# Kernel tuning notes

Hardware: AMD Instinct MI355X
Metric: run time of the kernel (lower is better)

## Reference

```python
import jax, jax.numpy as jnp
import numpy as np

QKV = 1024   # qkv_size (input feature dim)
E = 64       # embed_size (per-head dim)
H = 16       # num_heads
OUT = 1024   # output_size
B, S = 8, 1024


def setup_inputs() -> dict:
    key = jax.random.key(0)
    ks = jax.random.split(key, 8)
    inv = 1.0 / np.sqrt(QKV)
    return {
        "query": jax.random.normal(ks[0], (B, S, QKV), jnp.float32),
        "key": jax.random.normal(ks[1], (B, S, QKV), jnp.float32),
        "value": jax.random.normal(ks[2], (B, S, QKV), jnp.float32),
        # stacked per-head projection weights, torch Linear convention y = x @ W.T -> store as [H, QKV, E]
        "Wq": jax.random.normal(ks[3], (H, QKV, E), jnp.float32) * inv,
        "Wk": jax.random.normal(ks[4], (H, QKV, E), jnp.float32) * inv,
        "Wv": jax.random.normal(ks[5], (H, QKV, E), jnp.float32) * inv,
        "Wo": jax.random.normal(ks[6], (OUT, H * E), jnp.float32) / np.sqrt(H * E),
        "bo": jax.random.normal(ks[7], (OUT,), jnp.float32) * 0.01,
    }


def reference(query, key, value, Wq, Wk, Wv, Wo, bo):
    # batched over heads: [B,S,QKV] x [H,QKV,E] -> [B,H,S,E]
    Q = jnp.einsum("bsd,hde->bhse", query, Wq)
    K = jnp.einsum("bsd,hde->bhse", key, Wk)
    V = jnp.einsum("bsd,hde->bhse", value, Wv)
    # NOTE: original scales by sqrt(qkv_dim) (input dim), not per-head dim
    scale = 1.0 / jnp.sqrt(jnp.float32(QKV))
    scores = jnp.einsum("bhse,bhte->bhst", Q, K) * scale  # [B,H,S,S]
    attn = jax.nn.softmax(scores, axis=-1)
    attended = jnp.einsum("bhst,bhte->bhse", attn, V)     # [B,H,S,E]
    # concat heads along last dim (head-major order matches torch.cat of head outputs)
    concat = attended.transpose(0, 2, 1, 3).reshape(query.shape[0], query.shape[1], H * E)
    return concat @ Wo.T + bo
```

## Files before the change

### kernel.cpp

```cpp
#include <hip/hip_runtime.h>
#include <stdint.h>


typedef __bf16 bf16x8 __attribute__((ext_vector_type(8)));
typedef float f32x4 __attribute__((ext_vector_type(4)));

typedef __attribute__((address_space(3))) uint32_t lds_u32;
typedef const __attribute__((address_space(1))) uint32_t glb_u32;

__device__ __forceinline__ ushort f2bf(float f) {
  uint32_t x = __float_as_uint(f);
  x += 0x7fff + ((x >> 16) & 1);
  return (ushort)(x >> 16);
}
__device__ __forceinline__ bf16x8 ld8(const ushort* p) {
  union { uint4 u; bf16x8 b; } c;
  c.u = *reinterpret_cast<const uint4*>(p);
  return c.b;
}
__device__ __forceinline__ void cvt16(const float* __restrict__ src,
                                      ushort* __restrict__ dst) {
  union { uint4 u[2]; ushort s[16]; } o;
#pragma unroll
  for (int i = 0; i < 4; ++i) {
    const float4 f = reinterpret_cast<const float4*>(src)[i];
    o.s[4 * i + 0] = f2bf(f.x);
    o.s[4 * i + 1] = f2bf(f.y);
    o.s[4 * i + 2] = f2bf(f.z);
    o.s[4 * i + 3] = f2bf(f.w);
  }
  reinterpret_cast<uint4*>(dst)[0] = o.u[0];
  reinterpret_cast<uint4*>(dst)[1] = o.u[1];
}

__device__ __forceinline__ void gld16(const ushort* g, ushort* l) {
  __builtin_amdgcn_global_load_lds((glb_u32*)g, (lds_u32*)l, 16, 0, 0);
}

__global__ __launch_bounds__(256) void prep_wt(const float* __restrict__ W,
                                               ushort* __restrict__ WT) {
  __shared__ __align__(16) ushort tile[64 * 72];
  const int h = blockIdx.x >> 4;
  const int kt = blockIdx.x & 15;
  const int t = threadIdx.x;
  const int row = t >> 2;
  const int ch = (t & 3) * 16;
  cvt16(W + ((size_t)h * 1024 + kt * 64 + row) * 64 + ch, &tile[row * 72 + ch]);
  __syncthreads();
  const int e = t >> 2;
  const int kc = (t & 3) * 16;
  ushort vals[16];
#pragma unroll
  for (int j = 0; j < 16; ++j) vals[j] = tile[(kc + j) * 72 + e];
  ushort* dst = WT + (size_t)(h * 64 + e) * 1024 + kt * 64 + kc;
  reinterpret_cast<uint4*>(dst)[0] = *reinterpret_cast<uint4*>(&vals[0]);
  reinterpret_cast<uint4*>(dst)[1] = *reinterpret_cast<uint4*>(&vals[8]);
}

__global__ __launch_bounds__(256) void cvt_wo(const float* __restrict__ src,
                                              ushort* __restrict__ dst) {
  const int i = (blockIdx.x * 256 + threadIdx.x) * 16;
  cvt16(src + i, dst + i);
}

__global__ __launch_bounds__(256) void cvt2(const float* __restrict__ s0,
                                            ushort* __restrict__ d0,
                                            const float* __restrict__ s1,
                                            ushort* __restrict__ d1) {
  const int b = blockIdx.x;
  const float* s = (b < 2048) ? s0 : s1;
  ushort* d = (b < 2048) ? d0 : d1;
  const int i = ((b & 2047) * 256 + threadIdx.x) * 16;
  cvt16(s + i, d + i);
}

template <bool F32OUT>
__device__ __forceinline__ void gemm_core(const ushort* __restrict__ A,
                                          const ushort* __restrict__ Bt,
                                          const float* __restrict__ bias,
                                          void* __restrict__ Cv, float oscale,
                                          int bx, int by) {
  __shared__ __align__(16) ushort As[128 * 64];
  __shared__ __align__(16) ushort Bs[128 * 64];
  const int n0 = bx * 128;
  const int m0 = by * 128;
  const int t = threadIdx.x;
  const int lane = t & 63;
  const int w = t >> 6;
  const int wm = w >> 1, wn = w & 1;
  const int col = lane & 15;
  const int quad = lane >> 4;
  const int gr = lane >> 3;
  const int gc = (lane & 7) * 8;

  f32x4 acc[4][4];
#pragma unroll
  for (int i = 0; i < 4; ++i)
#pragma unroll
    for (int j = 0; j < 4; ++j) acc[i][j] = (f32x4){0.f, 0.f, 0.f, 0.f};

  const ushort* a_src = A + (size_t)(m0 + w * 8 + gr) * 1024 + gc;
  const ushort* b_src = Bt + (size_t)(n0 + w * 8 + gr) * 1024 + gc;
  ushort* as_base = &As[(w * 8) * 64];
  ushort* bs_base = &Bs[(w * 8) * 64];

  for (int k0 = 0; k0 < 1024; k0 += 64) {
#pragma unroll
    for (int c = 0; c < 4; ++c) {
      gld16(a_src + (size_t)c * 32 * 1024 + k0, as_base + c * 32 * 64);
      gld16(b_src + (size_t)c * 32 * 1024 + k0, bs_base + c * 32 * 64);
    }
    __syncthreads();

#pragma unroll
    for (int half = 0; half < 2; ++half) {
      bf16x8 af[4], bfr[4];
#pragma unroll
      for (int i = 0; i < 4; ++i)
        af[i] = ld8(&As[(wm * 64 + i * 16 + col) * 64 + half * 32 + quad * 8]);
#pragma unroll
      for (int j = 0; j < 4; ++j)
        bfr[j] = ld8(&Bs[(wn * 64 + j * 16 + col) * 64 + half * 32 + quad * 8]);
#pragma unroll
      for (int i = 0; i < 4; ++i)
#pragma unroll
        for (int j = 0; j < 4; ++j)
          acc[i][j] = __builtin_amdgcn_mfma_f32_16x16x32_bf16(af[i], bfr[j],
                                                              acc[i][j], 0, 0, 0);
    }
    __syncthreads();
  }

#pragma unroll
  for (int i = 0; i < 4; ++i)
#pragma unroll
    for (int j = 0; j < 4; ++j) {
      const int n = n0 + wn * 64 + j * 16 + col;
      float bv = 0.f;
      if (F32OUT) bv = bias[n];
#pragma unroll
      for (int r = 0; r < 4; ++r) {
        const int m = m0 + wm * 64 + i * 16 + quad * 4 + r;
        if (F32OUT)
          reinterpret_cast<float*>(Cv)[(size_t)m * 1024 + n] = acc[i][j][r] + bv;
        else
          reinterpret_cast<ushort*>(Cv)[(size_t)m * 1024 + n] =
              f2bf(acc[i][j][r] * oscale);
      }
    }
}

template <bool F32OUT>
__global__ __launch_bounds__(256) void gemm_bb(const ushort* __restrict__ A,
                                               const ushort* __restrict__ Bt,
                                               const float* __restrict__ bias,
                                               void* __restrict__ Cv,
                                               float oscale) {
  gemm_core<F32OUT>(A, Bt, bias, Cv, oscale, blockIdx.x, blockIdx.y);
}

__global__ __launch_bounds__(256) void gemm_proj2(
    const ushort* __restrict__ A0, const ushort* __restrict__ B0,
    ushort* __restrict__ C0, float s0, const ushort* __restrict__ A1,
    const ushort* __restrict__ B1, ushort* __restrict__ C1, float s1) {
  if (blockIdx.z == 0)
    gemm_core<false>(A0, B0, nullptr, C0, s0, blockIdx.x, blockIdx.y);
  else
    gemm_core<false>(A1, B1, nullptr, C1, s1, blockIdx.x, blockIdx.y);
}

__global__ __launch_bounds__(256) void flash_attn(const ushort* __restrict__ Q,
                                                  const ushort* __restrict__ K,
                                                  const ushort* __restrict__ V,
                                                  ushort* __restrict__ O) {
  __shared__ __align__(16) ushort QP[128 * 72];
  __shared__ __align__(16) ushort Ks[64 * 72];
  __shared__ __align__(16) ushort Vt[64 * 72];
  const int pair = blockIdx.x & 127;
  const int b = pair >> 4;
  const int h = pair & 15;
  const int qt = blockIdx.x >> 7;
  const int t = threadIdx.x;
  const int lane = t & 63;
  const int w = t >> 6;
  const int col = lane & 15;
  const int quad = lane >> 4;

  const size_t base = (size_t)b * 1024 * 1024 + h * 64;
  const int qrow0 = qt * 128;

  {
    const int row = t >> 1;
    const int c0 = (t & 1) * 32;
    const ushort* src = Q + base + (size_t)(qrow0 + row) * 1024 + c0;
    uint4 v0 = reinterpret_cast<const uint4*>(src)[0];
    uint4 v1 = reinterpret_cast<const uint4*>(src)[1];
    uint4 v2 = reinterpret_cast<const uint4*>(src)[2];
    uint4 v3 = reinterpret_cast<const uint4*>(src)[3];
    reinterpret_cast<uint4*>(&QP[row * 72 + c0])[0] = v0;
    reinterpret_cast<uint4*>(&QP[row * 72 + c0])[1] = v1;
    reinterpret_cast<uint4*>(&QP[row * 72 + c0])[2] = v2;
    reinterpret_cast<uint4*>(&QP[row * 72 + c0])[3] = v3;
  }
  __syncthreads();
  bf16x8 qa[2][2];
#pragma unroll
  for (int g = 0; g < 2; ++g)
#pragma unroll
    for (int half = 0; half < 2; ++half)
      qa[g][half] =
          ld8(&QP[(w * 32 + g * 16 + col) * 72 + half * 32 + quad * 8]);

  f32x4 o_[2][4];
#pragma unroll
  for (int g = 0; g < 2; ++g)
#pragma unroll
    for (int c = 0; c < 4; ++c) o_[g][c] = (f32x4){0.f, 0.f, 0.f, 0.f};
  float m_s[2] = {-1e30f, -1e30f};
  float l_s[2] = {0.f, 0.f};

  for (int kt = 0; kt < 16; ++kt) {
    {
      const int srow = t >> 2;
      const int sch = (t & 3) * 16;
      const ushort* ksrc = K + base + (size_t)(kt * 64 + srow) * 1024 + sch;
      uint4 kv0 = reinterpret_cast<const uint4*>(ksrc)[0];
      uint4 kv1 = reinterpret_cast<const uint4*>(ksrc)[1];
      const int vs = t & 63;
      const int ve = (t >> 6) * 16;
      const ushort* vsrc = V + base + (size_t)(kt * 64 + vs) * 1024 + ve;
      union { uint4 u[2]; ushort s[16]; } vv;
      vv.u[0] = reinterpret_cast<const uint4*>(vsrc)[0];
      vv.u[1] = reinterpret_cast<const uint4*>(vsrc)[1];
      reinterpret_cast<uint4*>(&Ks[srow * 72 + sch])[0] = kv0;
      reinterpret_cast<uint4*>(&Ks[srow * 72 + sch])[1] = kv1;
#pragma unroll
      for (int j = 0; j < 16; ++j) Vt[(ve + j) * 72 + vs] = vv.s[j];
    }
    __syncthreads();

    f32x4 sc[2][4];
#pragma unroll
    for (int c = 0; c < 4; ++c) {
      bf16x8 kb0 = ld8(&Ks[(c * 16 + col) * 72 + quad * 8]);
      bf16x8 kb1 = ld8(&Ks[(c * 16 + col) * 72 + 32 + quad * 8]);
#pragma unroll
      for (int g = 0; g < 2; ++g) {
        f32x4 z = {0.f, 0.f, 0.f, 0.f};
        z = __builtin_amdgcn_mfma_f32_16x16x32_bf16(kb0, qa[g][0], z, 0, 0, 0);
        z = __builtin_amdgcn_mfma_f32_16x16x32_bf16(kb1, qa[g][1], z, 0, 0, 0);
        sc[g][c] = z;
      }
    }

    float al[2];
#pragma unroll
    for (int g = 0; g < 2; ++g) {
      float mx = sc[g][0][0];
#pragma unroll
      for (int c = 0; c < 4; ++c)
#pragma unroll
        for (int r = 0; r < 4; ++r) mx = fmaxf(mx, sc[g][c][r]);
      mx = fmaxf(mx, __shfl_xor(mx, 16));
      mx = fmaxf(mx, __shfl_xor(mx, 32));
      const float m_new = fmaxf(m_s[g], mx);
      al[g] = __expf(m_s[g] - m_new);
      m_s[g] = m_new;
      float rs = 0.f;
      const int prow = (w * 32 + g * 16 + col) * 72;
#pragma unroll
      for (int c = 0; c < 4; ++c) {
        const float p0 = __expf(sc[g][c][0] - m_new);
        const float p1 = __expf(sc[g][c][1] - m_new);
        const float p2 = __expf(sc[g][c][2] - m_new);
        const float p3 = __expf(sc[g][c][3] - m_new);
        rs += (p0 + p1) + (p2 + p3);
        union { uint2 u; ushort s[4]; } pk;
        pk.s[0] = f2bf(p0);
        pk.s[1] = f2bf(p1);
        pk.s[2] = f2bf(p2);
        pk.s[3] = f2bf(p3);
        *reinterpret_cast<uint2*>(&QP[prow + c * 16 + quad * 4]) = pk.u;
      }
      rs += __shfl_xor(rs, 16);
      rs += __shfl_xor(rs, 32);
      l_s[g] = l_s[g] * al[g] + rs;
    }

#pragma unroll
    for (int g = 0; g < 2; ++g)
#pragma unroll
      for (int r = 0; r < 4; ++r) {
        const float a = __shfl(al[g], (lane & 48) | (quad * 4 + r));
        o_[g][0][r] *= a;
        o_[g][1][r] *= a;
        o_[g][2][r] *= a;
        o_[g][3][r] *= a;
      }

    bf16x8 pa[2][2];
#pragma unroll
    for (int g = 0; g < 2; ++g)
#pragma unroll
      for (int half = 0; half < 2; ++half)
        pa[g][half] =
            ld8(&QP[(w * 32 + g * 16 + col) * 72 + half * 32 + quad * 8]);
#pragma unroll
    for (int c = 0; c < 4; ++c) {
      bf16x8 vb0 = ld8(&Vt[(c * 16 + col) * 72 + quad * 8]);
      bf16x8 vb1 = ld8(&Vt[(c * 16 + col) * 72 + 32 + quad * 8]);
#pragma unroll
      for (int g = 0; g < 2; ++g) {
        o_[g][c] = __builtin_amdgcn_mfma_f32_16x16x32_bf16(pa[g][0], vb0,
                                                           o_[g][c], 0, 0, 0);
        o_[g][c] = __builtin_amdgcn_mfma_f32_16x16x32_bf16(pa[g][1], vb1,
                                                           o_[g][c], 0, 0, 0);
      }
    }
    __syncthreads();
  }

#pragma unroll
  for (int g = 0; g < 2; ++g)
#pragma unroll
    for (int r = 0; r < 4; ++r) {
      const float lr = __shfl(l_s[g], (lane & 48) | (quad * 4 + r));
      const float inv = 1.f / lr;
      const size_t row =
          base + (size_t)(qrow0 + w * 32 + g * 16 + quad * 4 + r) * 1024;
      O[row + 0 + col] = f2bf(o_[g][0][r] * inv);
      O[row + 16 + col] = f2bf(o_[g][1][r] * inv);
      O[row + 32 + col] = f2bf(o_[g][2][r] * inv);
      O[row + 48 + col] = f2bf(o_[g][3][r] * inv);
    }
}

extern "C" void kernel_launch(void* const* d_in, const int* in_sizes, int n_in,
                              void* d_out, int out_size, void* d_ws, size_t ws_size,
                              hipStream_t stream) {
  const float* q = (const float*)d_in[0];
  const float* k = (const float*)d_in[1];
  const float* v = (const float*)d_in[2];
  const float* Wq = (const float*)d_in[3];
  const float* Wk = (const float*)d_in[4];
  const float* Wv = (const float*)d_in[5];
  const float* Wo = (const float*)d_in[6];
  const float* bo = (const float*)d_in[7];
  float* out = (float*)d_out;
  ushort* ws = (ushort*)d_ws;

  const size_t M8 = 8u << 20;
  const size_t M1 = 1u << 20;
  ushort* Qp = ws;
  ushort* Kp = ws + M8;
  ushort* Vp = ws + 2 * M8;
  ushort* WqT = ws + 3 * M8;
  ushort* WkT = WqT + M1;
  ushort* WvT = WkT + M1;
  ushort* WoB = WvT + M1;

  ushort* X0 = (ushort*)d_out;
  ushort* X1 = X0 + M8;

  prep_wt<<<256, 256, 0, stream>>>(Wq, WqT);
  prep_wt<<<256, 256, 0, stream>>>(Wk, WkT);
  prep_wt<<<256, 256, 0, stream>>>(Wv, WvT);
  cvt_wo<<<256, 256, 0, stream>>>(Wo, WoB);

  cvt2<<<4096, 256, 0, stream>>>(q, X0, k, X1);
  gemm_proj2<<<dim3(8, 64, 2), 256, 0, stream>>>(X0, WqT, Qp, 0.03125f,
                                                 X1, WkT, Kp, 1.0f);
  cvt_wo<<<2048, 256, 0, stream>>>(v, X0);
  gemm_bb<false><<<dim3(8, 64), 256, 0, stream>>>(X0, WvT, nullptr, Vp, 1.0f);

  flash_attn<<<1024, 256, 0, stream>>>(Qp, Kp, Vp, Qp);

  gemm_bb<true><<<dim3(8, 64), 256, 0, stream>>>(Qp, WoB, bo, out, 1.0f);
}
```

Measured before the change: 355.8 us.

## Double-buffer GEMM LDS tiles, swizzle K tile loads, merge prep launches

```diff
diff --git a/kernel.cpp b/kernel.cpp
--- a/kernel.cpp
+++ b/kernel.cpp
@@ -37,11 +37,17 @@
   __builtin_amdgcn_global_load_lds((glb_u32*)g, (lds_u32*)l, 16, 0, 0);
 }
 
-__global__ __launch_bounds__(256) void prep_wt(const float* __restrict__ W,
-                                               ushort* __restrict__ WT) {
+__global__ __launch_bounds__(256) void prep_wt3(
+    const float* __restrict__ W0, const float* __restrict__ W1,
+    const float* __restrict__ W2, ushort* __restrict__ T0,
+    ushort* __restrict__ T1, ushort* __restrict__ T2) {
   __shared__ __align__(16) ushort tile[64 * 72];
-  const int h = blockIdx.x >> 4;
-  const int kt = blockIdx.x & 15;
+  const int sel = blockIdx.x >> 8;
+  const float* W = sel == 0 ? W0 : sel == 1 ? W1 : W2;
+  ushort* WT = sel == 0 ? T0 : sel == 1 ? T1 : T2;
+  const int bid = blockIdx.x & 255;
+  const int h = bid >> 4;
+  const int kt = bid & 15;
   const int t = threadIdx.x;
   const int row = t >> 2;
   const int ch = (t & 3) * 16;
@@ -63,15 +69,30 @@
   cvt16(src + i, dst + i);
 }
 
-__global__ __launch_bounds__(256) void cvt2(const float* __restrict__ s0,
+__global__ __launch_bounds__(256) void cvt3(const float* __restrict__ s0,
                                             ushort* __restrict__ d0,
                                             const float* __restrict__ s1,
-                                            ushort* __restrict__ d1) {
-  const int b = blockIdx.x;
-  const float* s = (b < 2048) ? s0 : s1;
-  ushort* d = (b < 2048) ? d0 : d1;
-  const int i = ((b & 2047) * 256 + threadIdx.x) * 16;
+                                            ushort* __restrict__ d1,
+                                            const float* __restrict__ s2,
+                                            ushort* __restrict__ d2) {
+  int b = blockIdx.x;
+  const float* s;
+  ushort* d;
+  if (b < 2048) { s = s0; d = d0; }
+  else if (b < 4096) { s = s1; d = d1; b -= 2048; }
+  else { s = s2; d = d2; b -= 4096; }
+  const int i = (b * 256 + threadIdx.x) * 16;
   cvt16(s + i, d + i);
+}
+
+__device__ __forceinline__ void stage_ab(const ushort* a_src,
+                                         const ushort* b_src, ushort* as,
+                                         ushort* bs, int w, int k0) {
+#pragma unroll
+  for (int c = 0; c < 4; ++c) {
+    gld16(a_src + (size_t)c * 32 * 1024 + k0, as + (w * 8 + c * 32) * 64);
+    gld16(b_src + (size_t)c * 32 * 1024 + k0, bs + (w * 8 + c * 32) * 64);
+  }
 }
 
 template <bool F32OUT>
@@ -80,8 +101,8 @@
                                           const float* __restrict__ bias,
                                           void* __restrict__ Cv, float oscale,
                                           int bx, int by) {
-  __shared__ __align__(16) ushort As[128 * 64];
-  __shared__ __align__(16) ushort Bs[128 * 64];
+  __shared__ __align__(16) ushort As[2][128 * 64];
+  __shared__ __align__(16) ushort Bs[2][128 * 64];
   const int n0 = bx * 128;
   const int m0 = by * 128;
   const int t = threadIdx.x;
@@ -101,26 +122,25 @@
 
   const ushort* a_src = A + (size_t)(m0 + w * 8 + gr) * 1024 + gc;
   const ushort* b_src = Bt + (size_t)(n0 + w * 8 + gr) * 1024 + gc;
-  ushort* as_base = &As[(w * 8) * 64];
-  ushort* bs_base = &Bs[(w * 8) * 64];
-
-  for (int k0 = 0; k0 < 1024; k0 += 64) {
-#pragma unroll
-    for (int c = 0; c < 4; ++c) {
-      gld16(a_src + (size_t)c * 32 * 1024 + k0, as_base + c * 32 * 64);
-      gld16(b_src + (size_t)c * 32 * 1024 + k0, bs_base + c * 32 * 64);
-    }
-    __syncthreads();
-
+
+  stage_ab(a_src, b_src, As[0], Bs[0], w, 0);
+  __syncthreads();
+
+  int cur = 0;
+  for (int it = 0; it < 16; ++it) {
+    if (it < 15)
+      stage_ab(a_src, b_src, As[cur ^ 1], Bs[cur ^ 1], w, (it + 1) * 64);
+    const ushort* asb = As[cur];
+    const ushort* bsb = Bs[cur];
 #pragma unroll
     for (int half = 0; half < 2; ++half) {
       bf16x8 af[4], bfr[4];
 #pragma unroll
       for (int i = 0; i < 4; ++i)
-        af[i] = ld8(&As[(wm * 64 + i * 16 + col) * 64 + half * 32 + quad * 8]);
+        af[i] = ld8(&asb[(wm * 64 + i * 16 + col) * 64 + half * 32 + quad * 8]);
 #pragma unroll
       for (int j = 0; j < 4; ++j)
-        bfr[j] = ld8(&Bs[(wn * 64 + j * 16 + col) * 64 + half * 32 + quad * 8]);
+        bfr[j] = ld8(&bsb[(wn * 64 + j * 16 + col) * 64 + half * 32 + quad * 8]);
 #pragma unroll
       for (int i = 0; i < 4; ++i)
 #pragma unroll
@@ -129,6 +149,7 @@
                                                               acc[i][j], 0, 0, 0);
     }
     __syncthreads();
+    cur ^= 1;
   }
 
 #pragma unroll
@@ -174,7 +195,7 @@
                                                   const ushort* __restrict__ V,
                                                   ushort* __restrict__ O) {
   __shared__ __align__(16) ushort QP[128 * 72];
-  __shared__ __align__(16) ushort Ks[64 * 72];
+  __shared__ __align__(16) ushort Ks[64 * 64];
   __shared__ __align__(16) ushort Vt[64 * 72];
   const int pair = blockIdx.x & 127;
   const int b = pair >> 4;
@@ -219,21 +240,21 @@
   float m_s[2] = {-1e30f, -1e30f};
   float l_s[2] = {0.f, 0.f};
 
+  const int krow = w * 16 + (lane >> 3);
+  const int kcs = (((lane & 7) ^ (lane >> 3)) << 3);
+  const int s7 = col & 7;
+
   for (int kt = 0; kt < 16; ++kt) {
     {
-      const int srow = t >> 2;
-      const int sch = (t & 3) * 16;
-      const ushort* ksrc = K + base + (size_t)(kt * 64 + srow) * 1024 + sch;
-      uint4 kv0 = reinterpret_cast<const uint4*>(ksrc)[0];
-      uint4 kv1 = reinterpret_cast<const uint4*>(ksrc)[1];
+      const ushort* k0 = K + base + (size_t)(kt * 64 + krow) * 1024 + kcs;
+      gld16(k0, &Ks[(w * 16) * 64]);
+      gld16(k0 + 8 * 1024, &Ks[(w * 16 + 8) * 64]);
       const int vs = t & 63;
       const int ve = (t >> 6) * 16;
       const ushort* vsrc = V + base + (size_t)(kt * 64 + vs) * 1024 + ve;
       union { uint4 u[2]; ushort s[16]; } vv;
       vv.u[0] = reinterpret_cast<const uint4*>(vsrc)[0];
       vv.u[1] = reinterpret_cast<const uint4*>(vsrc)[1];
-      reinterpret_cast<uint4*>(&Ks[srow * 72 + sch])[0] = kv0;
-      reinterpret_cast<uint4*>(&Ks[srow * 72 + sch])[1] = kv1;
 #pragma unroll
       for (int j = 0; j < 16; ++j) Vt[(ve + j) * 72 + vs] = vv.s[j];
     }
@@ -242,8 +263,9 @@
     f32x4 sc[2][4];
 #pragma unroll
     for (int c = 0; c < 4; ++c) {
-      bf16x8 kb0 = ld8(&Ks[(c * 16 + col) * 72 + quad * 8]);
-      bf16x8 kb1 = ld8(&Ks[(c * 16 + col) * 72 + 32 + quad * 8]);
+      const int R = (c * 16 + col) * 64;
+      bf16x8 kb0 = ld8(&Ks[R + ((quad ^ s7) << 3)]);
+      bf16x8 kb1 = ld8(&Ks[R + (((quad + 4) ^ s7) << 3)]);
 #pragma unroll
       for (int g = 0; g < 2; ++g) {
         f32x4 z = {0.f, 0.f, 0.f, 0.f};
@@ -362,12 +384,8 @@
   ushort* X0 = (ushort*)d_out;
   ushort* X1 = X0 + M8;
 
-  prep_wt<<<256, 256, 0, stream>>>(Wq, WqT);
-  prep_wt<<<256, 256, 0, stream>>>(Wk, WkT);
-  prep_wt<<<256, 256, 0, stream>>>(Wv, WvT);
-  cvt_wo<<<256, 256, 0, stream>>>(Wo, WoB);
-
-  cvt2<<<4096, 256, 0, stream>>>(q, X0, k, X1);
+  prep_wt3<<<768, 256, 0, stream>>>(Wq, Wk, Wv, WqT, WkT, WvT);
+  cvt3<<<4352, 256, 0, stream>>>(q, X0, k, X1, Wo, WoB);
   gemm_proj2<<<dim3(8, 64, 2), 256, 0, stream>>>(X0, WqT, Qp, 0.03125f,
                                                  X1, WkT, Kp, 1.0f);
   cvt_wo<<<2048, 256, 0, stream>>>(v, X0);
```

Result: slower. 384.4 us (+8.0%).
